# Kernel tuning notes

Measured on AMD Instinct MI355X. Metric: run time of the kernel, lower is better.

Reference implementation:

```python
import jax, jax.numpy as jnp
import numpy as np

D_MODEL = 1024
N_HEADS = 16
D_HEAD = D_MODEL // N_HEADS


def setup_inputs() -> dict:
    key = jax.random.key(0)
    ks = jax.random.split(key, 11)
    B, T = 2, 2048
    s = 1.0 / np.sqrt(D_MODEL)
    return {
        "query": jax.random.normal(ks[0], (B, T, D_MODEL), dtype=jnp.float32),
        "key": jax.random.normal(ks[1], (B, T, D_MODEL), dtype=jnp.float32),
        "value": jax.random.normal(ks[2], (B, T, D_MODEL), dtype=jnp.float32),
        "Wq": jax.random.normal(ks[3], (D_MODEL, D_MODEL), dtype=jnp.float32) * s,
        "bq": jnp.zeros((D_MODEL,), dtype=jnp.float32),
        "Wk": jax.random.normal(ks[4], (D_MODEL, D_MODEL), dtype=jnp.float32) * s,
        "bk": jnp.zeros((D_MODEL,), dtype=jnp.float32),
        "Wv": jax.random.normal(ks[5], (D_MODEL, D_MODEL), dtype=jnp.float32) * s,
        "bv": jnp.zeros((D_MODEL,), dtype=jnp.float32),
        "Wh": jax.random.normal(ks[6], (D_MODEL, D_MODEL), dtype=jnp.float32) * s,
        "bh": jnp.zeros((D_MODEL,), dtype=jnp.float32),
    }


def reference(query, key, value, Wq, bq, Wk, bk, Wv, bv, Wh, bh):
    B, T_src, _ = query.shape
    T_dst = key.shape[1]
    # torch nn.Linear: y = x @ W.T + b
    Q = query @ Wq.T + bq          # (B, T_src, D)
    K = key @ Wk.T + bk            # (B, T_dst, D)
    V = value @ Wv.T + bv          # (B, T_dst, D)
    Q = Q.reshape(B, T_src, N_HEADS, D_HEAD).transpose(0, 2, 1, 3)  # (B,H,Ts,dh)
    K = K.reshape(B, T_dst, N_HEADS, D_HEAD).transpose(0, 2, 1, 3)  # (B,H,Td,dh)
    V = V.reshape(B, T_dst, N_HEADS, D_HEAD).transpose(0, 2, 1, 3)  # (B,H,Td,dh)
    dot = jnp.einsum("bhsd,bhtd->bhst", Q, K) / np.sqrt(D_HEAD)     # (B,H,Ts,Td)
    scores = jax.nn.softmax(dot, axis=-1)
    out = jnp.einsum("bhst,bhtd->bhsd", scores, V)  # (B,H,Ts,dh)
    # Faithful to source: reshape WITHOUT transposing heads back (source quirk)
    out = out.reshape(B, T_src, D_MODEL)
    return out @ Wh.T + bh
```

## Files before the change

kernel.cpp:

```cpp
#include <hip/hip_runtime.h>
#include <hip/hip_bf16.h>
#include <stdint.h>

typedef __attribute__((ext_vector_type(8))) short bf16x8;
typedef __attribute__((ext_vector_type(4))) short bf16x4;
typedef __attribute__((ext_vector_type(4))) float f32x4;
typedef __attribute__((ext_vector_type(16))) float f32x16;
typedef __attribute__((ext_vector_type(4))) unsigned int u32x4;
typedef __attribute__((ext_vector_type(2))) __bf16 bf16x2n;

#define DEVI __device__ __forceinline__

DEVI short f2b(float f) {
  union { float f; uint32_t u; } x; x.f = f;
  uint32_t r = x.u + 0x7fffu + ((x.u >> 16) & 1u);
  return (short)(r >> 16);
}

DEVI unsigned packbf(float a, float b) {
  bf16x2n v; v[0] = (__bf16)a; v[1] = (__bf16)b;
  return __builtin_bit_cast(unsigned, v);
}

DEVI float exp2f_(float x) {
#if __has_builtin(__builtin_amdgcn_exp2f)
  return __builtin_amdgcn_exp2f(x);
#else
  return __expf(x * 0.6931471805599453f);
#endif
}

DEVI void plswap(unsigned& a, unsigned& b) {
#if __has_builtin(__builtin_amdgcn_permlane32_swap)
  auto r = __builtin_amdgcn_permlane32_swap(a, b, false, false);
  a = r[0]; b = r[1];
#else
  asm volatile("s_nop 1\n\tv_permlane32_swap_b32 %0, %1\n\ts_nop 1" : "+v"(a), "+v"(b));
#endif
}

DEVI float xmax32(float x) {
  unsigned a = __builtin_bit_cast(unsigned, x), b = a;
  plswap(a, b);
  return fmaxf(__builtin_bit_cast(float, a), __builtin_bit_cast(float, b));
}
DEVI float xsum32(float x) {
  unsigned a = __builtin_bit_cast(unsigned, x), b = a;
  plswap(a, b);
  return __builtin_bit_cast(float, a) + __builtin_bit_cast(float, b);
}

DEVI void async16(const void* gsrc, void* lds) {
  __builtin_amdgcn_global_load_lds((__attribute__((address_space(1))) void*)gsrc,
                                   (__attribute__((address_space(3))) void*)lds,
                                   16, 0, 0);
}

__global__ __launch_bounds__(256) void cvt_all(const float* __restrict__ q,
                                               const float* __restrict__ k,
                                               const float* __restrict__ v,
                                               const float* __restrict__ wq,
                                               const float* __restrict__ wk,
                                               const float* __restrict__ wv,
                                               const float* __restrict__ wh,
                                               short* __restrict__ ws) {
  const size_t MT = 4096ull * 1024ull;
  int bid = blockIdx.x;
  const float* src; short* dst; int idx;
  if (bid < 6144) {
    int r = bid >> 11;
    src = (r == 0) ? q : (r == 1) ? k : v;
    dst = ws + (size_t)r * MT;
    idx = (bid & 2047) * 256 + threadIdx.x;
  } else {
    int r = (bid - 6144) >> 9;
    src = (r == 0) ? wq : (r == 1) ? wk : (r == 2) ? wv : wh;
    dst = ws + 3 * MT + (size_t)r * (1024 * 1024);
    idx = ((bid - 6144) & 511) * 256 + threadIdx.x;
  }
  f32x4 a = ((const f32x4*)src)[2 * idx];
  f32x4 b = ((const f32x4*)src)[2 * idx + 1];
  bf16x8 o;
  o[0]=f2b(a[0]); o[1]=f2b(a[1]); o[2]=f2b(a[2]); o[3]=f2b(a[3]);
  o[4]=f2b(b[0]); o[5]=f2b(b[1]); o[6]=f2b(b[2]); o[7]=f2b(b[3]);
  ((bf16x8*)dst)[idx] = o;
}

__global__ __launch_bounds__(256) void gemm_qkv(const short* __restrict__ A0,
                                                const short* __restrict__ A1,
                                                const short* __restrict__ A2,
                                                const short* __restrict__ W0,
                                                const short* __restrict__ W1,
                                                const short* __restrict__ W2,
                                                const float* __restrict__ b0,
                                                const float* __restrict__ b1,
                                                const float* __restrict__ b2,
                                                short* __restrict__ O0,
                                                short* __restrict__ O1,
                                                short* __restrict__ O2) {
  constexpr int Kd = 1024, Nd = 1024;
  const int z = blockIdx.z;
  const short* A  = (z == 0) ? A0 : (z == 1) ? A1 : A2;
  const short* Bt = (z == 0) ? W0 : (z == 1) ? W1 : W2;
  const float* bias = (z == 0) ? b0 : (z == 1) ? b1 : b2;

  __shared__ __attribute__((aligned(128))) char smem[32768];
  char* As = smem;
  char* Bs = smem + 16384;
  const int tid = threadIdx.x, lane = tid & 63, wave = tid >> 6;
  const int m0 = blockIdx.x * 128, n0 = blockIdx.y * 128;
  const int wr = wave >> 1, wc = wave & 1;

  f32x4 acc[4][4];
#pragma unroll
  for (int i = 0; i < 4; i++)
#pragma unroll
    for (int j = 0; j < 4; j++) acc[i][j] = (f32x4)0.0f;

  for (int k0 = 0; k0 < Kd; k0 += 64) {
#pragma unroll
    for (int it = 0; it < 4; ++it) {
      int ci = it * 256 + tid;
      int r = ci >> 3, c8 = ci & 7;
      int sc = c8 ^ (r & 7);
      async16((const char*)A + ((size_t)(m0 + r) * Kd + k0) * 2 + sc * 16,
              As + it * 4096 + wave * 1024);
      async16((const char*)Bt + ((size_t)(n0 + r) * Kd + k0) * 2 + sc * 16,
              Bs + it * 4096 + wave * 1024);
    }
    __syncthreads();
#pragma unroll
    for (int kk = 0; kk < 2; ++kk) {
      bf16x8 af[4], bf[4];
#pragma unroll
      for (int i = 0; i < 4; i++) {
        int r = wr * 64 + i * 16 + (lane & 15);
        int cb = (kk * 64 + ((lane >> 4) << 4)) ^ ((r & 7) << 4);
        af[i] = *(const bf16x8*)(As + r * 128 + cb);
      }
#pragma unroll
      for (int j = 0; j < 4; j++) {
        int r = wc * 64 + j * 16 + (lane & 15);
        int cb = (kk * 64 + ((lane >> 4) << 4)) ^ ((r & 7) << 4);
        bf[j] = *(const bf16x8*)(Bs + r * 128 + cb);
      }
#pragma unroll
      for (int i = 0; i < 4; i++)
#pragma unroll
        for (int j = 0; j < 4; j++)
          acc[i][j] = __builtin_amdgcn_mfma_f32_16x16x32_bf16(af[i], bf[j], acc[i][j], 0, 0, 0);
    }
    __syncthreads();
  }

  const float scale = (z == 0) ? 0.18033688011112043f : 1.0f;
#pragma unroll
  for (int i = 0; i < 4; i++) {
    int mbase = m0 + wr * 64 + i * 16 + ((lane >> 4) << 2);
#pragma unroll
    for (int j = 0; j < 4; j++) {
      int n = n0 + wc * 64 + j * 16 + (lane & 15);
      float bvf = bias[n];
      if (z < 2) {
        short* out = (z == 0) ? O0 : O1;
#pragma unroll
        for (int r = 0; r < 4; r++)
          out[(size_t)(mbase + r) * Nd + n] = f2b((acc[i][j][r] + bvf) * scale);
      } else {
        int b = mbase >> 11, t = mbase & 2047;
        bf16x4 pk;
#pragma unroll
        for (int r = 0; r < 4; r++) pk[r] = f2b(acc[i][j][r] + bvf);
        *(bf16x4*)(O2 + ((size_t)(b * 1024 + n)) * 2048 + t) = pk;
      }
    }
  }
}

__global__ __launch_bounds__(256) void gemm_out(const short* __restrict__ A,
                                                const short* __restrict__ Bt,
                                                const float* __restrict__ bias,
                                                float* __restrict__ out) {
  constexpr int Kd = 1024, Nd = 1024;
  __shared__ __attribute__((aligned(128))) char smem[32768];
  char* As = smem;
  char* Bs = smem + 16384;
  const int tid = threadIdx.x, lane = tid & 63, wave = tid >> 6;
  const int m0 = blockIdx.x * 128, n0 = blockIdx.y * 128;
  const int wr = wave >> 1, wc = wave & 1;

  f32x4 acc[4][4];
#pragma unroll
  for (int i = 0; i < 4; i++)
#pragma unroll
    for (int j = 0; j < 4; j++) acc[i][j] = (f32x4)0.0f;

  for (int k0 = 0; k0 < Kd; k0 += 64) {
#pragma unroll
    for (int it = 0; it < 4; ++it) {
      int ci = it * 256 + tid;
      int r = ci >> 3, c8 = ci & 7;
      int sc = c8 ^ (r & 7);
      async16((const char*)A + ((size_t)(m0 + r) * Kd + k0) * 2 + sc * 16,
              As + it * 4096 + wave * 1024);
      async16((const char*)Bt + ((size_t)(n0 + r) * Kd + k0) * 2 + sc * 16,
              Bs + it * 4096 + wave * 1024);
    }
    __syncthreads();
#pragma unroll
    for (int kk = 0; kk < 2; ++kk) {
      bf16x8 af[4], bf[4];
#pragma unroll
      for (int i = 0; i < 4; i++) {
        int r = wr * 64 + i * 16 + (lane & 15);
        int cb = (kk * 64 + ((lane >> 4) << 4)) ^ ((r & 7) << 4);
        af[i] = *(const bf16x8*)(As + r * 128 + cb);
      }
#pragma unroll
      for (int j = 0; j < 4; j++) {
        int r = wc * 64 + j * 16 + (lane & 15);
        int cb = (kk * 64 + ((lane >> 4) << 4)) ^ ((r & 7) << 4);
        bf[j] = *(const bf16x8*)(Bs + r * 128 + cb);
      }
#pragma unroll
      for (int i = 0; i < 4; i++)
#pragma unroll
        for (int j = 0; j < 4; j++)
          acc[i][j] = __builtin_amdgcn_mfma_f32_16x16x32_bf16(af[i], bf[j], acc[i][j], 0, 0, 0);
    }
    __syncthreads();
  }

#pragma unroll
  for (int i = 0; i < 4; i++) {
    int mbase = m0 + wr * 64 + i * 16 + ((lane >> 4) << 2);
#pragma unroll
    for (int j = 0; j < 4; j++) {
      int n = n0 + wc * 64 + j * 16 + (lane & 15);
      float bvf = bias[n];
#pragma unroll
      for (int r = 0; r < 4; r++)
        out[(size_t)(mbase + r) * Nd + n] = acc[i][j][r] + bvf;
    }
  }
}

__global__ __launch_bounds__(256) void attn_kernel(const short* __restrict__ Q,
                                                   const short* __restrict__ K,
                                                   const short* __restrict__ Vt,
                                                   short* __restrict__ X) {
  constexpr int T = 2048, D = 1024;
  __shared__ __attribute__((aligned(128))) char smem[32768];
  const int tid = threadIdx.x, lane = tid & 63, wave = tid >> 6;
  const int hi1 = lane >> 5, l31 = lane & 31;

  int bid0 = blockIdx.x;
  int bid = (bid0 & 7) * 64 + (bid0 >> 3);
  const int bh = bid >> 4, qt = bid & 15;
  const int b = bh >> 4, h = bh & 15;
  const int qrow = qt * 128 + wave * 32 + l31;

  bf16x8 qf[4];
  {
    const short* qptr = Q + ((size_t)(b * T + qrow)) * D + h * 64 + hi1 * 8;
#pragma unroll
    for (int kk = 0; kk < 4; kk++) qf[kk] = *(const bf16x8*)(qptr + kk * 16);
  }

  f32x16 o0 = (f32x16)0.0f, o1 = (f32x16)0.0f;
  float m_run = -1e30f, l_run = 0.0f;

  auto STAGE = [&](int bufi, int t0) {
    char* Kd = smem + bufi * 8192;
    char* Vd = smem + 16384 + bufi * 8192;
#pragma unroll
    for (int it = 0; it < 2; ++it) {
      int ci = it * 256 + tid;
      int r = ci >> 3, c8 = ci & 7;
      int sc = (c8 ^ (r & 7)) * 16;
      async16((const char*)(K + ((size_t)(b * T + t0 + r)) * D + h * 64) + sc,
              Kd + it * 4096 + wave * 1024);
      async16((const char*)(Vt + ((size_t)(b * 1024 + h * 64 + r)) * T + t0) + sc,
              Vd + it * 4096 + wave * 1024);
    }
  };

  STAGE(0, 0);

  for (int it = 0; it < 32; ++it) {
    const int cur = it & 1;
    __syncthreads();
    if (it < 31) STAGE(cur ^ 1, (it + 1) * 64);

    char* Kb = smem + cur * 8192;
    char* Vb = smem + 16384 + cur * 8192;

    f32x16 s0 = (f32x16)0.0f, s1 = (f32x16)0.0f;
    __builtin_amdgcn_s_setprio(1);
#pragma unroll
    for (int kk = 0; kk < 4; kk++) {
      int cb = kk * 32 + hi1 * 16;
      bf16x8 ak0 = *(const bf16x8*)(Kb + l31 * 128 + (cb ^ ((l31 & 7) << 4)));
      s0 = __builtin_amdgcn_mfma_f32_32x32x16_bf16(ak0, qf[kk], s0, 0, 0, 0);
      bf16x8 ak1 = *(const bf16x8*)(Kb + (32 + l31) * 128 + (cb ^ ((l31 & 7) << 4)));
      s1 = __builtin_amdgcn_mfma_f32_32x32x16_bf16(ak1, qf[kk], s1, 0, 0, 0);
    }
    __builtin_amdgcn_s_setprio(0);

    float tm[16];
#pragma unroll
    for (int i = 0; i < 16; i++) tm[i] = fmaxf(s0[i], s1[i]);
#pragma unroll
    for (int st = 8; st > 0; st >>= 1)
#pragma unroll
      for (int i = 0; i < 16; i++) if (i < st) tm[i] = fmaxf(tm[i], tm[i + st]);
    float mall = xmax32(tm[0]);
    float mnew = fmaxf(m_run, mall);
    float corr = exp2f_(m_run - mnew);
    m_run = mnew;

    float ts[16];
#pragma unroll
    for (int i = 0; i < 16; i++) {
      float p0 = exp2f_(s0[i] - mnew);
      float p1 = exp2f_(s1[i] - mnew);
      s0[i] = p0; s1[i] = p1; ts[i] = p0 + p1;
    }
#pragma unroll
    for (int st = 8; st > 0; st >>= 1)
#pragma unroll
      for (int i = 0; i < 16; i++) if (i < st) ts[i] += ts[i + st];
    l_run = l_run * corr + xsum32(ts[0]);

#pragma unroll
    for (int i = 0; i < 16; i++) { o0[i] *= corr; o1[i] *= corr; }

    unsigned w[16];
#pragma unroll
    for (int r2 = 0; r2 < 4; r2++)
#pragma unroll
      for (int wi = 0; wi < 2; wi++) {
        w[r2 * 2 + wi]     = packbf(s0[r2 * 4 + 2 * wi], s0[r2 * 4 + 2 * wi + 1]);
        w[8 + r2 * 2 + wi] = packbf(s1[r2 * 4 + 2 * wi], s1[r2 * 4 + 2 * wi + 1]);
      }
    bf16x8 ap[4];
#pragma unroll
    for (int kk = 0; kk < 4; kk++) {
      u32x4 t4;
#pragma unroll
      for (int wi = 0; wi < 2; wi++) {
        unsigned a = w[(kk >> 1) * 8 + (kk & 1) * 4 + wi];
        unsigned c = w[(kk >> 1) * 8 + (kk & 1) * 4 + 2 + wi];
        plswap(a, c);
        t4[wi] = a; t4[2 + wi] = c;
      }
      ap[kk] = __builtin_bit_cast(bf16x8, t4);
    }

    __builtin_amdgcn_s_setprio(1);
#pragma unroll
    for (int kk = 0; kk < 4; kk++) {
      int cb = kk * 32 + hi1 * 16;
      bf16x8 av0 = *(const bf16x8*)(Vb + l31 * 128 + (cb ^ ((l31 & 7) << 4)));
      o0 = __builtin_amdgcn_mfma_f32_32x32x16_bf16(av0, ap[kk], o0, 0, 0, 0);
      bf16x8 av1 = *(const bf16x8*)(Vb + (32 + l31) * 128 + (cb ^ ((l31 & 7) << 4)));
      o1 = __builtin_amdgcn_mfma_f32_32x32x16_bf16(av1, ap[kk], o1, 0, 0, 0);
    }
    __builtin_amdgcn_s_setprio(0);
  }

  float inv = 1.0f / l_run;
  size_t xoff = ((size_t)(b * T + h * 128 + (qrow >> 4))) * D + ((qrow & 15) << 6) + hi1 * 4;
#pragma unroll
  for (int ntd = 0; ntd < 2; ntd++) {
#pragma unroll
    for (int rg = 0; rg < 4; rg++) {
      bf16x4 pk;
#pragma unroll
      for (int j = 0; j < 4; j++) {
        float v = (ntd == 0) ? o0[rg * 4 + j] : o1[rg * 4 + j];
        pk[j] = f2b(v * inv);
      }
      *(bf16x4*)(X + xoff + ntd * 32 + rg * 8) = pk;
    }
  }
}

extern "C" void kernel_launch(void* const* d_in, const int* in_sizes, int n_in,
                              void* d_out, int out_size, void* d_ws, size_t ws_size,
                              hipStream_t stream) {
  (void)in_sizes; (void)n_in; (void)out_size; (void)ws_size;
  const float* query = (const float*)d_in[0];
  const float* key   = (const float*)d_in[1];
  const float* value = (const float*)d_in[2];
  const float* Wq = (const float*)d_in[3];
  const float* bq = (const float*)d_in[4];
  const float* Wk = (const float*)d_in[5];
  const float* bk = (const float*)d_in[6];
  const float* Wv = (const float*)d_in[7];
  const float* bv = (const float*)d_in[8];
  const float* Wh = (const float*)d_in[9];
  const float* bh = (const float*)d_in[10];

  short* ws = (short*)d_ws;
  const size_t MT = 4096ull * 1024ull;
  short* qin_b = ws;
  short* kin_b = ws + MT;
  short* vin_b = ws + 2 * MT;
  short* Wq_b  = ws + 3 * MT;
  short* Wk_b  = Wq_b + 1024 * 1024;
  short* Wv_b  = Wk_b + 1024 * 1024;
  short* Wh_b  = Wv_b + 1024 * 1024;
  short* Qb    = ws + 4 * MT;
  short* Kb    = ws + 5 * MT;
  short* Vtb   = ws + 6 * MT;
  short* Xb    = ws + 7 * MT;

  cvt_all<<<8192, 256, 0, stream>>>(query, key, value, Wq, Wk, Wv, Wh, ws);

  gemm_qkv<<<dim3(32, 8, 3), 256, 0, stream>>>(qin_b, kin_b, vin_b,
                                               Wq_b, Wk_b, Wv_b,
                                               bq, bk, bv,
                                               Qb, Kb, Vtb);

  attn_kernel<<<512, 256, 0, stream>>>(Qb, Kb, Vtb, Xb);

  gemm_out<<<dim3(32, 8), 256, 0, stream>>>(Xb, Wh_b, bh, (float*)d_out);
}
```

Measured before the change: 141.2 us.

## Halve attention block size and add lazy softmax rescaling with deferred row sums

The attention kernel now runs 128-thread blocks with 64 query rows each, launched as 1024 blocks, so the grid has more, smaller blocks. The online softmax only rescales the accumulators when some lane's max exceeds the running max by more than 8 (in the exp2 domain). The per-row sum is kept as a per-lane vector and reduced across lanes once at the end rather than every iteration. Together these cut the per-iteration cross-lane reductions and rescale multiplies. In exchange, each block reuses its staged K/V tiles for only half as many query rows, and letting the running max lag by up to 8 can push exp values as high as 256 before conversion to bf16.

```diff
diff --git a/kernel.cpp b/kernel.cpp
--- a/kernel.cpp
+++ b/kernel.cpp
@@ -245,7 +245,7 @@
   }
 }
 
-__global__ __launch_bounds__(256) void attn_kernel(const short* __restrict__ Q,
+__global__ __launch_bounds__(128) void attn_kernel(const short* __restrict__ Q,
                                                    const short* __restrict__ K,
                                                    const short* __restrict__ Vt,
                                                    short* __restrict__ X) {
@@ -255,10 +255,10 @@
   const int hi1 = lane >> 5, l31 = lane & 31;
 
   int bid0 = blockIdx.x;
-  int bid = (bid0 & 7) * 64 + (bid0 >> 3);
-  const int bh = bid >> 4, qt = bid & 15;
+  int bid = (bid0 & 7) * 128 + (bid0 >> 3);
+  const int bh = bid >> 5, qt = bid & 31;
   const int b = bh >> 4, h = bh & 15;
-  const int qrow = qt * 128 + wave * 32 + l31;
+  const int qrow = qt * 64 + wave * 32 + l31;
 
   bf16x8 qf[4];
   {
@@ -268,20 +268,24 @@
   }
 
   f32x16 o0 = (f32x16)0.0f, o1 = (f32x16)0.0f;
-  float m_run = -1e30f, l_run = 0.0f;
+  f32x16 lvec = (f32x16)0.0f;
+  float m_run = -1e30f;
+
+  const int swz = (l31 & 7) << 4;
+  const int rK0 = l31 * 128, rK1 = (32 + l31) * 128;
 
   auto STAGE = [&](int bufi, int t0) {
     char* Kd = smem + bufi * 8192;
     char* Vd = smem + 16384 + bufi * 8192;
 #pragma unroll
-    for (int it = 0; it < 2; ++it) {
-      int ci = it * 256 + tid;
+    for (int it = 0; it < 4; ++it) {
+      int ci = it * 128 + tid;
       int r = ci >> 3, c8 = ci & 7;
       int sc = (c8 ^ (r & 7)) * 16;
       async16((const char*)(K + ((size_t)(b * T + t0 + r)) * D + h * 64) + sc,
-              Kd + it * 4096 + wave * 1024);
+              Kd + it * 2048 + wave * 1024);
       async16((const char*)(Vt + ((size_t)(b * 1024 + h * 64 + r)) * T + t0) + sc,
-              Vd + it * 4096 + wave * 1024);
+              Vd + it * 2048 + wave * 1024);
     }
   };
 
@@ -299,41 +303,39 @@
     __builtin_amdgcn_s_setprio(1);
 #pragma unroll
     for (int kk = 0; kk < 4; kk++) {
-      int cb = kk * 32 + hi1 * 16;
-      bf16x8 ak0 = *(const bf16x8*)(Kb + l31 * 128 + (cb ^ ((l31 & 7) << 4)));
+      int cb = (kk * 32 + hi1 * 16) ^ swz;
+      bf16x8 ak0 = *(const bf16x8*)(Kb + rK0 + cb);
       s0 = __builtin_amdgcn_mfma_f32_32x32x16_bf16(ak0, qf[kk], s0, 0, 0, 0);
-      bf16x8 ak1 = *(const bf16x8*)(Kb + (32 + l31) * 128 + (cb ^ ((l31 & 7) << 4)));
+      bf16x8 ak1 = *(const bf16x8*)(Kb + rK1 + cb);
       s1 = __builtin_amdgcn_mfma_f32_32x32x16_bf16(ak1, qf[kk], s1, 0, 0, 0);
     }
     __builtin_amdgcn_s_setprio(0);
 
-    float tm[16];
-#pragma unroll
-    for (int i = 0; i < 16; i++) tm[i] = fmaxf(s0[i], s1[i]);
-#pragma unroll
-    for (int st = 8; st > 0; st >>= 1)
-#pragma unroll
-      for (int i = 0; i < 16; i++) if (i < st) tm[i] = fmaxf(tm[i], tm[i + st]);
-    float mall = xmax32(tm[0]);
-    float mnew = fmaxf(m_run, mall);
-    float corr = exp2f_(m_run - mnew);
-    m_run = mnew;
-
-    float ts[16];
+    float t8[8];
+#pragma unroll
+    for (int i = 0; i < 8; i++)
+      t8[i] = fmaxf(fmaxf(s0[i], s0[i + 8]), fmaxf(s1[i], s1[i + 8]));
+    float ta = fmaxf(fmaxf(t8[0], t8[1]), t8[2]);
+    float tb = fmaxf(fmaxf(t8[3], t8[4]), t8[5]);
+    float tm = fmaxf(fmaxf(t8[6], t8[7]), fmaxf(ta, tb));
+
+    if (!__all(tm <= m_run + 8.0f)) {
+      float mnew = fmaxf(m_run, xmax32(tm));
+      float corr = exp2f_(m_run - mnew);
+      m_run = mnew;
+#pragma unroll
+      for (int i = 0; i < 16; i++) {
+        lvec[i] *= corr; o0[i] *= corr; o1[i] *= corr;
+      }
+    }
+
 #pragma unroll
     for (int i = 0; i < 16; i++) {
-      float p0 = exp2f_(s0[i] - mnew);
-      float p1 = exp2f_(s1[i] - mnew);
-      s0[i] = p0; s1[i] = p1; ts[i] = p0 + p1;
-    }
-#pragma unroll
-    for (int st = 8; st > 0; st >>= 1)
-#pragma unroll
-      for (int i = 0; i < 16; i++) if (i < st) ts[i] += ts[i + st];
-    l_run = l_run * corr + xsum32(ts[0]);
-
-#pragma unroll
-    for (int i = 0; i < 16; i++) { o0[i] *= corr; o1[i] *= corr; }
+      float p0 = exp2f_(s0[i] - m_run);
+      float p1 = exp2f_(s1[i] - m_run);
+      s0[i] = p0; s1[i] = p1;
+      lvec[i] += p0 + p1;
+    }
 
     unsigned w[16];
 #pragma unroll
@@ -360,16 +362,22 @@
     __builtin_amdgcn_s_setprio(1);
 #pragma unroll
     for (int kk = 0; kk < 4; kk++) {
-      int cb = kk * 32 + hi1 * 16;
-      bf16x8 av0 = *(const bf16x8*)(Vb + l31 * 128 + (cb ^ ((l31 & 7) << 4)));
+      int cb = (kk * 32 + hi1 * 16) ^ swz;
+      bf16x8 av0 = *(const bf16x8*)(Vb + rK0 + cb);
       o0 = __builtin_amdgcn_mfma_f32_32x32x16_bf16(av0, ap[kk], o0, 0, 0, 0);
-      bf16x8 av1 = *(const bf16x8*)(Vb + (32 + l31) * 128 + (cb ^ ((l31 & 7) << 4)));
+      bf16x8 av1 = *(const bf16x8*)(Vb + rK1 + cb);
       o1 = __builtin_amdgcn_mfma_f32_32x32x16_bf16(av1, ap[kk], o1, 0, 0, 0);
     }
     __builtin_amdgcn_s_setprio(0);
   }
 
+  float l0 = (lvec[0] + lvec[1]) + (lvec[2] + lvec[3]);
+  float l1 = (lvec[4] + lvec[5]) + (lvec[6] + lvec[7]);
+  float l2 = (lvec[8] + lvec[9]) + (lvec[10] + lvec[11]);
+  float l3 = (lvec[12] + lvec[13]) + (lvec[14] + lvec[15]);
+  float l_run = xsum32((l0 + l1) + (l2 + l3));
   float inv = 1.0f / l_run;
+
   size_t xoff = ((size_t)(b * T + h * 128 + (qrow >> 4))) * D + ((qrow & 15) << 6) + hi1 * 4;
 #pragma unroll
   for (int ntd = 0; ntd < 2; ntd++) {
@@ -423,7 +431,7 @@
                                                bq, bk, bv,
                                                Qb, Kb, Vtb);
 
-  attn_kernel<<<512, 256, 0, stream>>>(Qb, Kb, Vtb, Xb);
+  attn_kernel<<<1024, 128, 0, stream>>>(Qb, Kb, Vtb, Xb);
 
   gemm_out<<<dim3(32, 8), 256, 0, stream>>>(Xb, Wh_b, bh, (float*)d_out);
 }
```

New measurement: 139.5 us. No clear change (-1.2%).
